# Kernel optimization log

Measured on AMD Instinct MI355X. Metric: run time of the kernel, lower is better.

The kernel has to match this reference:

```python
import jax, jax.numpy as jnp
import numpy as np
from jax import lax

K = 3
STRIDE = 1
PAD = 1


def setup_inputs() -> dict:
    key = jax.random.key(0)
    k0, k1, k2, k3 = jax.random.split(key, 4)
    B, C, H, W, O = 8, 128, 64, 64, 128
    x = jax.random.normal(k0, (B, C, H, W), jnp.float32)
    # offset_conv: Conv2d(C, 2*K*K) - small init so sampled offsets stay moderate
    w_off = jax.random.normal(k1, (2 * K * K, C, K, K), jnp.float32) * 0.01
    b_off = jnp.zeros((2 * K * K,), jnp.float32)
    # deform_conv main weight, kaiming-ish scale
    w_def = jax.random.normal(k2, (O, C, K, K), jnp.float32) * (1.0 / np.sqrt(C * K * K))
    b_def = jax.random.normal(k3, (O,), jnp.float32) * 0.01
    return {"x": x, "w_off": w_off, "b_off": b_off, "w_def": w_def, "b_def": b_def}


def _conv2d(x, w, b, stride, pad):
    y = lax.conv_general_dilated(
        x, w, window_strides=(stride, stride), padding=[(pad, pad), (pad, pad)],
        dimension_numbers=("NCHW", "OIHW", "NCHW"))
    return y + b[None, :, None, None]


def _bilinear_sample(x, py, px):
    """x: [B,C,Hin,Win]; py,px: [B,KK,H,W] -> [B,C,KK,H,W] with zero padding."""
    B, C, Hin, Win = x.shape
    iy0f = jnp.floor(py)
    ix0f = jnp.floor(px)
    wy = py - iy0f  # grad of floor is 0, so d(wy)/d(py) = 1 (matches deform conv)
    wx = px - ix0f
    iy0 = iy0f.astype(jnp.int32)
    ix0 = ix0f.astype(jnp.int32)

    def gather(iy, ix):
        valid = (iy >= 0) & (iy < Hin) & (ix >= 0) & (ix < Win)
        iyc = jnp.clip(iy, 0, Hin - 1)
        ixc = jnp.clip(ix, 0, Win - 1)
        g = jax.vmap(lambda xb, a, b: xb[:, a, b])(x, iyc, ixc)  # [B,C,KK,H,W]
        return g * valid[:, None].astype(x.dtype)

    v00 = gather(iy0, ix0)
    v01 = gather(iy0, ix0 + 1)
    v10 = gather(iy0 + 1, ix0)
    v11 = gather(iy0 + 1, ix0 + 1)
    wy_ = wy[:, None]
    wx_ = wx[:, None]
    return (v00 * (1 - wy_) * (1 - wx_) + v01 * (1 - wy_) * wx_
            + v10 * wy_ * (1 - wx_) + v11 * wy_ * wx_)


def reference(x, w_off, b_off, w_def, b_def):
    B, C, H, W = x.shape
    O = w_def.shape[0]
    KK = K * K
    # 1) standard conv predicting offsets: [B, 2*KK, Hout, Wout]
    offsets = _conv2d(x, w_off, b_off, STRIDE, PAD)
    Hout, Wout = offsets.shape[2], offsets.shape[3]
    # torchvision layout: interleaved (dy, dx) per kernel tap
    off = offsets.reshape(B, KK, 2, Hout, Wout)
    off_y, off_x = off[:, :, 0], off[:, :, 1]  # [B,KK,Hout,Wout]
    # 2) base sampling grid per kernel tap
    kys, kxs = jnp.meshgrid(jnp.arange(K), jnp.arange(K), indexing="ij")
    kys = kys.reshape(KK).astype(jnp.float32)
    kxs = kxs.reshape(KK).astype(jnp.float32)
    hs = (jnp.arange(Hout) * STRIDE - PAD).astype(jnp.float32)
    ws = (jnp.arange(Wout) * STRIDE - PAD).astype(jnp.float32)
    base_y = hs[None, :, None] + kys[:, None, None]  # [KK,Hout,1]
    base_x = ws[None, None, :] + kxs[:, None, None]  # [KK,1,Wout]
    py = base_y[None] + off_y  # [B,KK,Hout,Wout]
    px = base_x[None] + off_x
    # 3) gather bilinear-sampled patches then dense contraction (im2col GEMM)
    sampled = _bilinear_sample(x, py, px)  # [B,C,KK,Hout,Wout]
    out = jnp.einsum("bckhw,ock->bohw", sampled, w_def.reshape(O, C, KK))
    return out + b_def[None, :, None, None]
```

## Files before the change

### kernel.cpp

```cpp
#include <hip/hip_runtime.h>
#include <hip/hip_bf16.h>

#define BB 8
#define CC 128
#define HH 64
#define WW 64
#define OO 128
#define NJ 18
#define HW 4096

typedef unsigned short u16;
typedef unsigned int u32;
typedef __attribute__((ext_vector_type(8))) __bf16 bf16x8;
typedef __attribute__((ext_vector_type(4))) float f32x4;

__device__ __forceinline__ u16 f2bf(float f) {
    u32 u = __float_as_uint(f);
    u += 0x7fffu + ((u >> 16) & 1u);
    return (u16)(u >> 16);
}
__device__ __forceinline__ float bflo(u32 u) { return __uint_as_float(u << 16); }
__device__ __forceinline__ float bfhi(u32 u) { return __uint_as_float(u & 0xffff0000u); }
__device__ __forceinline__ u32 pk2bf(float s0, float s1) {
    union { __hip_bfloat162 h; u32 u; } cv;
    cv.h = __float22bfloat162_rn(make_float2(s0, s1));
    return cv.u;
}

__global__ __launch_bounds__(256)
void k_pre(const float* __restrict__ x, u16* __restrict__ xT,
           const float* __restrict__ w_def, const float* __restrict__ w_off,
           u16* __restrict__ wT, u16* __restrict__ wA) {
    __shared__ float tile[64][129];
    const int t = threadIdx.x;
    if (blockIdx.x < 512) {
        const int b = blockIdx.x >> 6;
        const int hw0 = (blockIdx.x & 63) << 6;
        const float* xb = x + (size_t)b * CC * HW + hw0;
        const int tw = t & 63, tc = t >> 6;
#pragma unroll
        for (int r = 0; r < 32; ++r) {
            int c = r * 4 + tc;
            tile[tw][c] = xb[c * HW + tw];
        }
        __syncthreads();
        u16* dst = xT + ((size_t)b * HW + hw0) * CC;
#pragma unroll
        for (int r = 0; r < 4; ++r) {
            int item = t + (r << 8);
            int seg = item & 15, hw = item >> 4;
            union { u32 d[4]; uint4 v; } p;
#pragma unroll
            for (int i = 0; i < 4; ++i)
                p.d[i] = pk2bf(tile[hw][seg * 8 + 2 * i], tile[hw][seg * 8 + 2 * i + 1]);
            *(uint4*)&dst[hw * CC + seg * 8] = p.v;
        }
    } else {
        int idx = (blockIdx.x - 512) * 256 + t;
        if (idx < 9 * OO * CC) {
            int c = idx & 127, o = (idx >> 7) & 127, kk = idx >> 14;
            wT[idx] = f2bf(w_def[(o * CC + c) * 9 + kk]);
        }
        if (idx < 32 * 1152) {
            int k = idx % 1152, j = idx / 1152;
            int q = k >> 7, c = k & 127;
            wA[idx] = (j < NJ) ? f2bf(w_off[(j * CC + c) * 9 + q]) : (u16)0;
        }
    }
}

__global__ __launch_bounds__(256, 2)
void k_fused(const u16* __restrict__ xT, const u16* __restrict__ wA,
             const float* __restrict__ b_off, const u16* __restrict__ wT,
             const float* __restrict__ b_def, float* __restrict__ out) {
    __shared__ __align__(16) u16 smem[25344];
    u16*   s_x    = smem;
    float* s_off  = (float*)smem;
    u16*   s_samp = smem + 4096;

    const int t = threadIdx.x, lane = t & 63, wv = t >> 6;
    const int posl = lane & 15, kg = lane >> 4;
    const int b = blockIdx.x & 7, h = blockIdx.x >> 3;
    const char* xb = (const char*)xT + (size_t)b * (HW * CC * 2);

    for (int it = t; it < 3168; it += 256) {
        int seg = it & 15, pix = it >> 4;
        int r = pix / 66, wp = pix - r * 66;
        int y = h - 1 + r, w = wp - 1;
        uint4 v = make_uint4(0, 0, 0, 0);
        if (y >= 0 && y < HH && w >= 0 && w < WW)
            v = *(const uint4*)&xT[((size_t)(b * HW) + y * WW + w) * CC + seg * 8];
        *(uint4*)&s_x[pix * 128 + ((seg ^ (pix & 15)) * 8)] = v;
    }
    __syncthreads();

    {
        f32x4 acc0 = {0.f, 0.f, 0.f, 0.f}, acc1 = {0.f, 0.f, 0.f, 0.f};
        for (int qq = 0; qq < 9; ++qq) {
            int qy = qq / 3, qx = qq - qy * 3;
            int pix = qy * 66 + (wv * 16 + posl) + qx;
            int prow = pix * 128, pxr = pix & 15;
#pragma unroll
            for (int ki = 0; ki < 4; ++ki) {
                int ks = qq * 4 + ki;
                int cidx = ki * 4 + kg;
                bf16x8 bfr = *(const bf16x8*)&s_x[prow + ((cidx ^ pxr) * 8)];
                bf16x8 a0 = *(const bf16x8*)&wA[posl * 1152 + ks * 32 + kg * 8];
                bf16x8 a1 = *(const bf16x8*)&wA[(16 + posl) * 1152 + ks * 32 + kg * 8];
                acc0 = __builtin_amdgcn_mfma_f32_16x16x32_bf16(a0, bfr, acc0, 0, 0, 0);
                acc1 = __builtin_amdgcn_mfma_f32_16x16x32_bf16(a1, bfr, acc1, 0, 0, 0);
            }
        }
        __syncthreads();
        const int pos = wv * 16 + posl;
#pragma unroll
        for (int r = 0; r < 4; ++r) {
            int j = kg * 4 + r;
            s_off[j * 64 + pos] = acc0[r] + b_off[j];
        }
#pragma unroll
        for (int r = 0; r < 4; ++r) {
            int j = 16 + kg * 4 + r;
            if (j < NJ) s_off[j * 64 + pos] = acc1[r] + b_off[j];
        }
    }
    __syncthreads();

    const int gpos = t >> 2;
    const int segsub = t & 3;
    const int pxor = gpos & 15;
    const int slotbase = gpos * 128;

    float oyv[9], oxv[9];
#pragma unroll
    for (int kk = 0; kk < 9; ++kk) {
        oyv[kk] = s_off[(2 * kk) * 64 + gpos];
        oxv[kk] = s_off[(2 * kk + 1) * 64 + gpos];
    }

    auto coords = [&](int kk, float oy, float ox, float4& cw, int4& co) {
        int ky = kk / 3, kx = kk - ky * 3;
        float py = (float)(h - 1 + ky) + oy;
        float px = (float)(gpos - 1 + kx) + ox;
        float fy = floorf(py), fx = floorf(px);
        int iy0 = (int)fy, ix0 = (int)fx;
        float wy = py - fy, wx = px - fx;
        int iy1 = iy0 + 1, ix1 = ix0 + 1;
        float my0 = (iy0 >= 0 && iy0 < HH) ? 1.0f : 0.0f;
        float my1 = (iy1 >= 0 && iy1 < HH) ? 1.0f : 0.0f;
        float mx0 = (ix0 >= 0 && ix0 < WW) ? 1.0f : 0.0f;
        float mx1 = (ix1 >= 0 && ix1 < WW) ? 1.0f : 0.0f;
        int iy0c = min(max(iy0, 0), HH - 1), iy1c = min(max(iy1, 0), HH - 1);
        int ix0c = min(max(ix0, 0), WW - 1), ix1c = min(max(ix1, 0), WW - 1);
        float wy1 = 1.0f - wy, wx1 = 1.0f - wx;
        cw = make_float4(my0 * mx0 * wy1 * wx1, my0 * mx1 * wy1 * wx,
                         my1 * mx0 * wy  * wx1, my1 * mx1 * wy  * wx);
        co = make_int4((iy0c * WW + ix0c) << 8, (iy0c * WW + ix1c) << 8,
                       (iy1c * WW + ix0c) << 8, (iy1c * WW + ix1c) << 8);
    };
    auto issue_gather = [&](const int4 co, uint4 q[4][4]) {
#pragma unroll
        for (int j = 0; j < 4; ++j) {
            const int sb = (segsub + 4 * j) * 16;
            q[j][0] = *(const uint4*)(xb + co.x + sb);
            q[j][1] = *(const uint4*)(xb + co.y + sb);
            q[j][2] = *(const uint4*)(xb + co.z + sb);
            q[j][3] = *(const uint4*)(xb + co.w + sb);
        }
    };
    auto interp_store = [&](const float4 cw, uint4 q[4][4], int p) {
#pragma unroll
        for (int j = 0; j < 4; ++j) {
            const int seg = segsub + 4 * j;
            const u32* u00 = (const u32*)&q[j][0];
            const u32* u01 = (const u32*)&q[j][1];
            const u32* u10 = (const u32*)&q[j][2];
            const u32* u11 = (const u32*)&q[j][3];
            union { u32 d[4]; uint4 v; } pk;
#pragma unroll
            for (int i = 0; i < 4; ++i) {
                float s0 = cw.x * bflo(u00[i]) + cw.y * bflo(u01[i])
                         + cw.z * bflo(u10[i]) + cw.w * bflo(u11[i]);
                float s1 = cw.x * bfhi(u00[i]) + cw.y * bfhi(u01[i])
                         + cw.z * bfhi(u10[i]) + cw.w * bfhi(u11[i]);
                pk.d[i] = pk2bf(s0, s1);
            }
            *(uint4*)&s_samp[p * 8192 + slotbase + ((seg ^ pxor) * 8)] = pk.v;
        }
    };
    auto load_w = [&](int kk, bf16x8 wfr[4][2]) {
        const u16* wkk = wT + kk * (OO * CC);
        const int o0 = wv * 32;
#pragma unroll
        for (int ct = 0; ct < 4; ++ct)
#pragma unroll
            for (int nt = 0; nt < 2; ++nt) {
                int o = o0 + nt * 16 + posl;
                wfr[ct][nt] = *(const bf16x8*)&wkk[o * CC + ct * 32 + kg * 8];
            }
    };

    f32x4 acc[4][2];
#pragma unroll
    for (int mt = 0; mt < 4; ++mt) {
        acc[mt][0] = (f32x4){0.f, 0.f, 0.f, 0.f};
        acc[mt][1] = (f32x4){0.f, 0.f, 0.f, 0.f};
    }

    bf16x8 wA_[4][2], wB_[4][2];
    float4 cw; int4 co;
    uint4 q[4][4];
    load_w(0, wA_);
    coords(0, oyv[0], oxv[0], cw, co);
    issue_gather(co, q);
    interp_store(cw, q, 0);
    __syncthreads();

#pragma unroll
    for (int kk = 0; kk < 9; ++kk) {
        const int p = kk & 1;

        if (kk < 8) {
            load_w(kk + 1, wB_);
            coords(kk + 1, oyv[kk + 1], oxv[kk + 1], cw, co);
            issue_gather(co, q);
        }

#pragma unroll
        for (int ct = 0; ct < 4; ++ct) {
            const int chunk = ct * 4 + kg;
#pragma unroll
            for (int mt = 0; mt < 4; ++mt) {
                bf16x8 afr = *(const bf16x8*)
                    &s_samp[p * 8192 + (mt * 16 + posl) * 128 + ((chunk ^ posl) * 8)];
                acc[mt][0] = __builtin_amdgcn_mfma_f32_16x16x32_bf16(
                    afr, wA_[ct][0], acc[mt][0], 0, 0, 0);
                acc[mt][1] = __builtin_amdgcn_mfma_f32_16x16x32_bf16(
                    afr, wA_[ct][1], acc[mt][1], 0, 0, 0);
            }
        }

        if (kk < 8) {
            interp_store(cw, q, p ^ 1);
            __syncthreads();
        }

#pragma unroll
        for (int ct = 0; ct < 4; ++ct) {
            wA_[ct][0] = wB_[ct][0];
            wA_[ct][1] = wB_[ct][1];
        }
    }

#pragma unroll
    for (int nt = 0; nt < 2; ++nt) {
        const int o = wv * 32 + nt * 16 + posl;
        const float bd = b_def[o];
        float* orow = out + ((b * OO + o) * HH + h) * WW;
#pragma unroll
        for (int mt = 0; mt < 4; ++mt) {
            float4 res;
            res.x = acc[mt][nt][0] + bd;
            res.y = acc[mt][nt][1] + bd;
            res.z = acc[mt][nt][2] + bd;
            res.w = acc[mt][nt][3] + bd;
            *(float4*)&orow[mt * 16 + kg * 4] = res;
        }
    }
}

extern "C" void kernel_launch(void* const* d_in, const int* in_sizes, int n_in,
                              void* d_out, int out_size, void* d_ws, size_t ws_size,
                              hipStream_t stream) {
    const float* x     = (const float*)d_in[0];
    const float* w_off = (const float*)d_in[1];
    const float* b_off = (const float*)d_in[2];
    const float* w_def = (const float*)d_in[3];
    const float* b_def = (const float*)d_in[4];
    float* out = (float*)d_out;

    u16* xT = (u16*)d_ws;
    u16* wT = xT + (size_t)BB * HW * CC;
    u16* wA = wT + 9 * OO * CC;

    k_pre  <<<1088, 256, 0, stream>>>(x, xT, w_def, w_off, wT, wA);
    k_fused<<< 512, 256, 0, stream>>>(xT, wA, b_off, wT, b_def, out);
}
```

Baseline: 128.1 us.

## Double fused kernel block size to 512 threads and split work across 8 waves

The fused deformable-conv kernel now runs with 512 threads per block instead of 256. The offset-conv MFMA is split so each wave computes one 16-row group of offset channels. Each thread gathers half as many channel segments, and the main GEMM splits the M tiles across two wave groups. The goal is more waves in flight to hide gather latency and cut per-thread register use. The cost is redundant weight-fragment loads, since both wave groups load the same W tiles, plus heavier barrier synchronization across more waves.

```diff
diff --git a/kernel.cpp b/kernel.cpp
--- a/kernel.cpp
+++ b/kernel.cpp
@@ -69,7 +69,7 @@
     }
 }
 
-__global__ __launch_bounds__(256, 2)
+__global__ __launch_bounds__(512, 4)
 void k_fused(const u16* __restrict__ xT, const u16* __restrict__ wA,
              const float* __restrict__ b_off, const u16* __restrict__ wT,
              const float* __restrict__ b_def, float* __restrict__ out) {
@@ -83,7 +83,7 @@
     const int b = blockIdx.x & 7, h = blockIdx.x >> 3;
     const char* xb = (const char*)xT + (size_t)b * (HW * CC * 2);
 
-    for (int it = t; it < 3168; it += 256) {
+    for (int it = t; it < 3168; it += 512) {
         int seg = it & 15, pix = it >> 4;
         int r = pix / 66, wp = pix - r * 66;
         int y = h - 1 + r, w = wp - 1;
@@ -95,41 +95,37 @@
     __syncthreads();
 
     {
-        f32x4 acc0 = {0.f, 0.f, 0.f, 0.f}, acc1 = {0.f, 0.f, 0.f, 0.f};
+        const int jg = wv >> 2, wq = wv & 3;
+        f32x4 acc0 = {0.f, 0.f, 0.f, 0.f};
         for (int qq = 0; qq < 9; ++qq) {
             int qy = qq / 3, qx = qq - qy * 3;
-            int pix = qy * 66 + (wv * 16 + posl) + qx;
+            int pix = qy * 66 + (wq * 16 + posl) + qx;
             int prow = pix * 128, pxr = pix & 15;
 #pragma unroll
             for (int ki = 0; ki < 4; ++ki) {
                 int ks = qq * 4 + ki;
                 int cidx = ki * 4 + kg;
                 bf16x8 bfr = *(const bf16x8*)&s_x[prow + ((cidx ^ pxr) * 8)];
-                bf16x8 a0 = *(const bf16x8*)&wA[posl * 1152 + ks * 32 + kg * 8];
-                bf16x8 a1 = *(const bf16x8*)&wA[(16 + posl) * 1152 + ks * 32 + kg * 8];
+                bf16x8 a0 = *(const bf16x8*)&wA[(jg * 16 + posl) * 1152 + ks * 32 + kg * 8];
                 acc0 = __builtin_amdgcn_mfma_f32_16x16x32_bf16(a0, bfr, acc0, 0, 0, 0);
-                acc1 = __builtin_amdgcn_mfma_f32_16x16x32_bf16(a1, bfr, acc1, 0, 0, 0);
             }
         }
         __syncthreads();
-        const int pos = wv * 16 + posl;
+        const int pos = wq * 16 + posl;
 #pragma unroll
         for (int r = 0; r < 4; ++r) {
-            int j = kg * 4 + r;
-            s_off[j * 64 + pos] = acc0[r] + b_off[j];
-        }
-#pragma unroll
-        for (int r = 0; r < 4; ++r) {
-            int j = 16 + kg * 4 + r;
-            if (j < NJ) s_off[j * 64 + pos] = acc1[r] + b_off[j];
+            int j = jg * 16 + kg * 4 + r;
+            if (j < NJ) s_off[j * 64 + pos] = acc0[r] + b_off[j];
         }
     }
     __syncthreads();
 
-    const int gpos = t >> 2;
-    const int segsub = t & 3;
+    const int gpos = t >> 3;
+    const int segsub = t & 7;
     const int pxor = gpos & 15;
     const int slotbase = gpos * 128;
+    const int mgrp = wv >> 2;
+    const int wvn = wv & 3;
 
     float oyv[9], oxv[9];
 #pragma unroll
@@ -158,20 +154,20 @@
         co = make_int4((iy0c * WW + ix0c) << 8, (iy0c * WW + ix1c) << 8,
                        (iy1c * WW + ix0c) << 8, (iy1c * WW + ix1c) << 8);
     };
-    auto issue_gather = [&](const int4 co, uint4 q[4][4]) {
-#pragma unroll
-        for (int j = 0; j < 4; ++j) {
-            const int sb = (segsub + 4 * j) * 16;
+    auto issue_gather = [&](const int4 co, uint4 q[2][4]) {
+#pragma unroll
+        for (int j = 0; j < 2; ++j) {
+            const int sb = (segsub + 8 * j) * 16;
             q[j][0] = *(const uint4*)(xb + co.x + sb);
             q[j][1] = *(const uint4*)(xb + co.y + sb);
             q[j][2] = *(const uint4*)(xb + co.z + sb);
             q[j][3] = *(const uint4*)(xb + co.w + sb);
         }
     };
-    auto interp_store = [&](const float4 cw, uint4 q[4][4], int p) {
-#pragma unroll
-        for (int j = 0; j < 4; ++j) {
-            const int seg = segsub + 4 * j;
+    auto interp_store = [&](const float4 cw, uint4 q[2][4], int p) {
+#pragma unroll
+        for (int j = 0; j < 2; ++j) {
+            const int seg = segsub + 8 * j;
             const u32* u00 = (const u32*)&q[j][0];
             const u32* u01 = (const u32*)&q[j][1];
             const u32* u10 = (const u32*)&q[j][2];
@@ -190,7 +186,7 @@
     };
     auto load_w = [&](int kk, bf16x8 wfr[4][2]) {
         const u16* wkk = wT + kk * (OO * CC);
-        const int o0 = wv * 32;
+        const int o0 = wvn * 32;
 #pragma unroll
         for (int ct = 0; ct < 4; ++ct)
 #pragma unroll
@@ -200,16 +196,16 @@
             }
     };
 
-    f32x4 acc[4][2];
-#pragma unroll
-    for (int mt = 0; mt < 4; ++mt) {
-        acc[mt][0] = (f32x4){0.f, 0.f, 0.f, 0.f};
-        acc[mt][1] = (f32x4){0.f, 0.f, 0.f, 0.f};
+    f32x4 acc[2][2];
+#pragma unroll
+    for (int mtl = 0; mtl < 2; ++mtl) {
+        acc[mtl][0] = (f32x4){0.f, 0.f, 0.f, 0.f};
+        acc[mtl][1] = (f32x4){0.f, 0.f, 0.f, 0.f};
     }
 
     bf16x8 wA_[4][2], wB_[4][2];
     float4 cw; int4 co;
-    uint4 q[4][4];
+    uint4 q[2][4];
     load_w(0, wA_);
     coords(0, oyv[0], oxv[0], cw, co);
     issue_gather(co, q);
@@ -230,13 +226,14 @@
         for (int ct = 0; ct < 4; ++ct) {
             const int chunk = ct * 4 + kg;
 #pragma unroll
-            for (int mt = 0; mt < 4; ++mt) {
+            for (int mtl = 0; mtl < 2; ++mtl) {
+                const int mt = mgrp * 2 + mtl;
                 bf16x8 afr = *(const bf16x8*)
                     &s_samp[p * 8192 + (mt * 16 + posl) * 128 + ((chunk ^ posl) * 8)];
-                acc[mt][0] = __builtin_amdgcn_mfma_f32_16x16x32_bf16(
-                    afr, wA_[ct][0], acc[mt][0], 0, 0, 0);
-                acc[mt][1] = __builtin_amdgcn_mfma_f32_16x16x32_bf16(
-                    afr, wA_[ct][1], acc[mt][1], 0, 0, 0);
+                acc[mtl][0] = __builtin_amdgcn_mfma_f32_16x16x32_bf16(
+                    afr, wA_[ct][0], acc[mtl][0], 0, 0, 0);
+                acc[mtl][1] = __builtin_amdgcn_mfma_f32_16x16x32_bf16(
+                    afr, wA_[ct][1], acc[mtl][1], 0, 0, 0);
             }
         }
 
@@ -254,16 +251,17 @@
 
 #pragma unroll
     for (int nt = 0; nt < 2; ++nt) {
-        const int o = wv * 32 + nt * 16 + posl;
+        const int o = wvn * 32 + nt * 16 + posl;
         const float bd = b_def[o];
         float* orow = out + ((b * OO + o) * HH + h) * WW;
 #pragma unroll
-        for (int mt = 0; mt < 4; ++mt) {
+        for (int mtl = 0; mtl < 2; ++mtl) {
+            const int mt = mgrp * 2 + mtl;
             float4 res;
-            res.x = acc[mt][nt][0] + bd;
-            res.y = acc[mt][nt][1] + bd;
-            res.z = acc[mt][nt][2] + bd;
-            res.w = acc[mt][nt][3] + bd;
+            res.x = acc[mtl][nt][0] + bd;
+            res.y = acc[mtl][nt][1] + bd;
+            res.z = acc[mtl][nt][2] + bd;
+            res.w = acc[mtl][nt][3] + bd;
             *(float4*)&orow[mt * 16 + kg * 4] = res;
         }
     }
@@ -284,5 +282,5 @@
     u16* wA = wT + 9 * OO * CC;
 
     k_pre  <<<1088, 256, 0, stream>>>(x, xT, w_def, w_off, wT, wA);
-    k_fused<<< 512, 256, 0, stream>>>(xT, wA, b_off, wT, b_def, out);
-}
+    k_fused<<< 512, 512, 0, stream>>>(xT, wA, b_off, wT, b_def, out);
+}
```

New measurement: 139.5 us, median of 2. 1.09x slower.

## Feed bilinear samples straight into MFMA registers, dropping shared-memory staging

Applied to the files above, without the earlier changes.

Each wave now gathers and interpolates its own 16 pixels directly into MFMA A-fragments and multiplies them against all 128 output channels. This removes the double-buffered shared-memory sample tile and the per-tap barriers. In exchange, every wave reloads the full weight slice for each tap from global/L2 (four times the weight traffic), and the software pipeline that overlapped the next tap's gather with the current MFMAs is gone.

```diff
diff --git a/kernel.cpp b/kernel.cpp
--- a/kernel.cpp
+++ b/kernel.cpp
@@ -74,9 +74,8 @@
              const float* __restrict__ b_off, const u16* __restrict__ wT,
              const float* __restrict__ b_def, float* __restrict__ out) {
     __shared__ __align__(16) u16 smem[25344];
-    u16*   s_x    = smem;
-    float* s_off  = (float*)smem;
-    u16*   s_samp = smem + 4096;
+    u16*   s_x   = smem;
+    float* s_off = (float*)smem;
 
     const int t = threadIdx.x, lane = t & 63, wv = t >> 6;
     const int posl = lane & 15, kg = lane >> 4;
@@ -126,10 +125,8 @@
     }
     __syncthreads();
 
-    const int gpos = t >> 2;
-    const int segsub = t & 3;
-    const int pxor = gpos & 15;
-    const int slotbase = gpos * 128;
+    const int p0 = wv * 16;
+    const int gpos = p0 + posl;
 
     float oyv[9], oxv[9];
 #pragma unroll
@@ -158,25 +155,34 @@
         co = make_int4((iy0c * WW + ix0c) << 8, (iy0c * WW + ix1c) << 8,
                        (iy1c * WW + ix0c) << 8, (iy1c * WW + ix1c) << 8);
     };
-    auto issue_gather = [&](const int4 co, uint4 q[4][4]) {
-#pragma unroll
-        for (int j = 0; j < 4; ++j) {
-            const int sb = (segsub + 4 * j) * 16;
-            q[j][0] = *(const uint4*)(xb + co.x + sb);
-            q[j][1] = *(const uint4*)(xb + co.y + sb);
-            q[j][2] = *(const uint4*)(xb + co.z + sb);
-            q[j][3] = *(const uint4*)(xb + co.w + sb);
-        }
-    };
-    auto interp_store = [&](const float4 cw, uint4 q[4][4], int p) {
-#pragma unroll
-        for (int j = 0; j < 4; ++j) {
-            const int seg = segsub + 4 * j;
-            const u32* u00 = (const u32*)&q[j][0];
-            const u32* u01 = (const u32*)&q[j][1];
-            const u32* u10 = (const u32*)&q[j][2];
-            const u32* u11 = (const u32*)&q[j][3];
-            union { u32 d[4]; uint4 v; } pk;
+
+    f32x4 acc[8];
+#pragma unroll
+    for (int ot = 0; ot < 8; ++ot) acc[ot] = (f32x4){0.f, 0.f, 0.f, 0.f};
+
+#pragma unroll
+    for (int kk = 0; kk < 9; ++kk) {
+        float4 cw; int4 co;
+        coords(kk, oyv[kk], oxv[kk], cw, co);
+
+        uint4 g[4][4];
+#pragma unroll
+        for (int ks = 0; ks < 4; ++ks) {
+            const int sb = ks * 64 + kg * 16;
+            g[ks][0] = *(const uint4*)(xb + co.x + sb);
+            g[ks][1] = *(const uint4*)(xb + co.y + sb);
+            g[ks][2] = *(const uint4*)(xb + co.z + sb);
+            g[ks][3] = *(const uint4*)(xb + co.w + sb);
+        }
+
+        bf16x8 A[4];
+#pragma unroll
+        for (int ks = 0; ks < 4; ++ks) {
+            const u32* u00 = (const u32*)&g[ks][0];
+            const u32* u01 = (const u32*)&g[ks][1];
+            const u32* u10 = (const u32*)&g[ks][2];
+            const u32* u11 = (const u32*)&g[ks][3];
+            union { u32 d[4]; bf16x8 v; } pk;
 #pragma unroll
             for (int i = 0; i < 4; ++i) {
                 float s0 = cw.x * bflo(u00[i]) + cw.y * bflo(u01[i])
@@ -185,87 +191,30 @@
                          + cw.z * bfhi(u10[i]) + cw.w * bfhi(u11[i]);
                 pk.d[i] = pk2bf(s0, s1);
             }
-            *(uint4*)&s_samp[p * 8192 + slotbase + ((seg ^ pxor) * 8)] = pk.v;
-        }
-    };
-    auto load_w = [&](int kk, bf16x8 wfr[4][2]) {
+            A[ks] = pk.v;
+        }
+
         const u16* wkk = wT + kk * (OO * CC);
-        const int o0 = wv * 32;
-#pragma unroll
-        for (int ct = 0; ct < 4; ++ct)
-#pragma unroll
-            for (int nt = 0; nt < 2; ++nt) {
-                int o = o0 + nt * 16 + posl;
-                wfr[ct][nt] = *(const bf16x8*)&wkk[o * CC + ct * 32 + kg * 8];
+#pragma unroll
+        for (int ks = 0; ks < 4; ++ks)
+#pragma unroll
+            for (int ot = 0; ot < 8; ++ot) {
+                bf16x8 wfr = *(const bf16x8*)&wkk[(ot * 16 + posl) * CC + ks * 32 + kg * 8];
+                acc[ot] = __builtin_amdgcn_mfma_f32_16x16x32_bf16(
+                    A[ks], wfr, acc[ot], 0, 0, 0);
             }
-    };
-
-    f32x4 acc[4][2];
-#pragma unroll
-    for (int mt = 0; mt < 4; ++mt) {
-        acc[mt][0] = (f32x4){0.f, 0.f, 0.f, 0.f};
-        acc[mt][1] = (f32x4){0.f, 0.f, 0.f, 0.f};
-    }
-
-    bf16x8 wA_[4][2], wB_[4][2];
-    float4 cw; int4 co;
-    uint4 q[4][4];
-    load_w(0, wA_);
-    coords(0, oyv[0], oxv[0], cw, co);
-    issue_gather(co, q);
-    interp_store(cw, q, 0);
-    __syncthreads();
-
-#pragma unroll
-    for (int kk = 0; kk < 9; ++kk) {
-        const int p = kk & 1;
-
-        if (kk < 8) {
-            load_w(kk + 1, wB_);
-            coords(kk + 1, oyv[kk + 1], oxv[kk + 1], cw, co);
-            issue_gather(co, q);
-        }
-
-#pragma unroll
-        for (int ct = 0; ct < 4; ++ct) {
-            const int chunk = ct * 4 + kg;
-#pragma unroll
-            for (int mt = 0; mt < 4; ++mt) {
-                bf16x8 afr = *(const bf16x8*)
-                    &s_samp[p * 8192 + (mt * 16 + posl) * 128 + ((chunk ^ posl) * 8)];
-                acc[mt][0] = __builtin_amdgcn_mfma_f32_16x16x32_bf16(
-                    afr, wA_[ct][0], acc[mt][0], 0, 0, 0);
-                acc[mt][1] = __builtin_amdgcn_mfma_f32_16x16x32_bf16(
-                    afr, wA_[ct][1], acc[mt][1], 0, 0, 0);
-            }
-        }
-
-        if (kk < 8) {
-            interp_store(cw, q, p ^ 1);
-            __syncthreads();
-        }
-
-#pragma unroll
-        for (int ct = 0; ct < 4; ++ct) {
-            wA_[ct][0] = wB_[ct][0];
-            wA_[ct][1] = wB_[ct][1];
-        }
-    }
-
-#pragma unroll
-    for (int nt = 0; nt < 2; ++nt) {
-        const int o = wv * 32 + nt * 16 + posl;
+    }
+
+#pragma unroll
+    for (int ot = 0; ot < 8; ++ot) {
+        const int o = ot * 16 + posl;
         const float bd = b_def[o];
-        float* orow = out + ((b * OO + o) * HH + h) * WW;
-#pragma unroll
-        for (int mt = 0; mt < 4; ++mt) {
-            float4 res;
-            res.x = acc[mt][nt][0] + bd;
-            res.y = acc[mt][nt][1] + bd;
-            res.z = acc[mt][nt][2] + bd;
-            res.w = acc[mt][nt][3] + bd;
-            *(float4*)&orow[mt * 16 + kg * 4] = res;
-        }
+        float4 res;
+        res.x = acc[ot][0] + bd;
+        res.y = acc[ot][1] + bd;
+        res.z = acc[ot][2] + bd;
+        res.w = acc[ot][3] + bd;
+        *(float4*)&out[((b * OO + o) * HH + h) * WW + p0 + kg * 4] = res;
     }
 }
 
```

New measurement: 192.4 us. 50.2% more time.
